# Performance work log

Measured on AMD Instinct MI355X. Metric: run time of the kernel, lower is better.

The kernel has to match this reference:

```python
import jax, jax.numpy as jnp
import numpy as np

P = 64  # number of parameters per grid cell
# torch.combinations(param, 2, with_replacement=True) enumerates (i,j) with i<=j
# in row-major order, which matches np.triu_indices.
IDX_I, IDX_J = np.triu_indices(P)  # each length C = P*(P+1)//2 = 2080


def setup_inputs() -> dict:
    key = jax.random.key(0)
    k1, k2 = jax.random.split(key)
    # [B, G1, G2, P]
    param_tensor = jax.random.normal(k1, (32, 64, 64, P), dtype=jnp.float32)
    # [G1, G2, C]
    coeffs = jax.random.normal(k2, (64, 64, len(IDX_I)), dtype=jnp.float32)
    return {"param_tensor": param_tensor, "coeffs": coeffs}


def reference(param_tensor, coeffs):
    # Pairwise products with replacement: p_i * p_j for i <= j  -> [B,G1,G2,C]
    pair = param_tensor[..., IDX_I] * param_tensor[..., IDX_J]
    # Per-cell weighted sum over combinations, then sum over the 2D grid -> [B]
    cell = jnp.einsum('bijc,ijc->bij', pair, coeffs)
    return cell.sum(axis=(1, 2))
```

## Files before the change

kernel.cpp:

```cpp
#include <hip/hip_runtime.h>

#define NP     64
#define NC     2080
#define NCELLS 4096
#define NB     32
#define CELLS_PER_BLOCK 4
#define BLOCKS (NCELLS / CELLS_PER_BLOCK)
#define CSTRIDE 2112

typedef short bf16x8  __attribute__((ext_vector_type(8)));
typedef short short4v __attribute__((ext_vector_type(4)));
typedef float f32x16  __attribute__((ext_vector_type(16)));

__device__ __forceinline__ short f2bf(float f) {
  unsigned u = __float_as_uint(f);
  u += 0x7fffu + ((u >> 16) & 1u);
  return (short)(u >> 16);
}

__global__ __launch_bounds__(256, 4) void poly_mfma_kernel(
    const float* __restrict__ param,
    const float* __restrict__ coeffs,
    float* __restrict__ ws) {
  __shared__ short scoefh[CELLS_PER_BLOCK][CSTRIDE];
  __shared__ float sred[CELLS_PER_BLOCK][NB];

  const int tid  = threadIdx.x;
  const int wave = tid >> 6;
  const int lane = tid & 63;
  const int lo5  = lane & 31;
  const int hi   = lane >> 5;
  const int cellbase = blockIdx.x * CELLS_PER_BLOCK;
  const int cell = cellbase + wave;

  {
    const float4* gsrc =
        reinterpret_cast<const float4*>(coeffs + (size_t)cellbase * NC);
#pragma unroll
    for (int k = 0; k < 9; ++k) {
      const int idx = tid + k * 256;
      if (idx < (CELLS_PER_BLOCK * NC) / 4) {
        const int cl = idx / 520;
        const int q  = idx - cl * 520;
        const float4 v = gsrc[idx];
        short4v h;
        h[0] = f2bf(v.x); h[1] = f2bf(v.y);
        h[2] = f2bf(v.z); h[3] = f2bf(v.w);
        *reinterpret_cast<short4v*>(&scoefh[cl][4 * q]) = h;
      }
    }
  }

  const float* pb = param + ((size_t)lo5 * NCELLS + cell) * NP;
  bf16x8 afrag[4];
#pragma unroll
  for (int ks = 0; ks < 4; ++ks) {
#pragma unroll
    for (int eh = 0; eh < 2; ++eh) {
      const int i0 = ks * 16 + 4 * hi + 8 * eh;
      const float4 v = *reinterpret_cast<const float4*>(pb + i0);
      afrag[ks][eh * 4 + 0] = f2bf(v.x);
      afrag[ks][eh * 4 + 1] = f2bf(v.y);
      afrag[ks][eh * 4 + 2] = f2bf(v.z);
      afrag[ks][eh * 4 + 3] = f2bf(v.w);
    }
  }

  __syncthreads();

  float pepi0[16], pepi1[16];
#pragma unroll
  for (int r = 0; r < 16; ++r) {
    const int b = (r & 3) + 8 * (r >> 2) + 4 * hi;
    const float* pe = param + ((size_t)b * NCELLS + cell) * NP;
    pepi0[r] = pe[lo5];
    pepi1[r] = pe[lo5 + 32];
  }

  const short* sw = &scoefh[wave][0];
  f32x16 acc0, acc1;
#pragma unroll
  for (int r = 0; r < 16; ++r) { acc0[r] = 0.f; acc1[r] = 0.f; }

#pragma unroll
  for (int ks = 0; ks < 4; ++ks) {
    bf16x8 b0, b1;
#pragma unroll
    for (int e = 0; e < 8; ++e) {
      const int i = ks * 16 + 4 * hi + (e & 3) + 8 * (e >> 2);
      const int cbase = i * (127 - i) / 2;
      const short v0 = sw[cbase + lo5];
      const short v1 = sw[cbase + lo5 + 32];
      b0[e] = (lo5 >= i) ? v0 : (short)0;
      b1[e] = (lo5 + 32 >= i) ? v1 : (short)0;
    }
    acc0 = __builtin_amdgcn_mfma_f32_32x32x16_bf16(afrag[ks], b0, acc0, 0, 0, 0);
    acc1 = __builtin_amdgcn_mfma_f32_32x32x16_bf16(afrag[ks], b1, acc1, 0, 0, 0);
  }

  float dacc[16];
#pragma unroll
  for (int r = 0; r < 16; ++r)
    dacc[r] = fmaf(acc0[r], pepi0[r], acc1[r] * pepi1[r]);

#pragma unroll
  for (int r = 0; r < 16; ++r) {
    float v = dacc[r];
    v += __shfl_xor(v, 1, 64);
    v += __shfl_xor(v, 2, 64);
    v += __shfl_xor(v, 4, 64);
    v += __shfl_xor(v, 8, 64);
    v += __shfl_xor(v, 16, 64);
    dacc[r] = v;
  }
  if (lo5 == 0) {
#pragma unroll
    for (int r = 0; r < 16; ++r) {
      const int b = (r & 3) + 8 * (r >> 2) + 4 * hi;
      sred[wave][b] = dacc[r];
    }
  }
  __syncthreads();
  if (tid < NB) {
    ws[(size_t)tid * BLOCKS + blockIdx.x] =
        sred[0][tid] + sred[1][tid] + sred[2][tid] + sred[3][tid];
  }
}

__global__ void poly_reduce_kernel(const float* __restrict__ ws,
                                   float* __restrict__ out) {
  const int b = blockIdx.x;
  const int tid = threadIdx.x;
  const float4 v =
      reinterpret_cast<const float4*>(ws + (size_t)b * BLOCKS)[tid];
  float s = (v.x + v.y) + (v.z + v.w);
#pragma unroll
  for (int off = 1; off <= 32; off <<= 1) s += __shfl_xor(s, off, 64);
  __shared__ float sp[4];
  if ((tid & 63) == 0) sp[tid >> 6] = s;
  __syncthreads();
  if (tid == 0) out[b] = (sp[0] + sp[1]) + (sp[2] + sp[3]);
}

extern "C" void kernel_launch(void* const* d_in, const int* in_sizes, int n_in,
                              void* d_out, int out_size, void* d_ws,
                              size_t ws_size, hipStream_t stream) {
  const float* param = (const float*)d_in[0];
  const float* coeffs = (const float*)d_in[1];
  float* out = (float*)d_out;
  float* ws = (float*)d_ws;

  hipLaunchKernelGGL(poly_mfma_kernel, dim3(BLOCKS), dim3(256), 0, stream,
                     param, coeffs, ws);
  hipLaunchKernelGGL(poly_reduce_kernel, dim3(NB), dim3(256), 0, stream, ws,
                     out);
}
```

Before: 22.30 us.

## Store coefficients as swizzled transposed upper-triangular matrix and use DPP reductions

Each wave now loads only its own cell's coefficients into a zero-initialised, XOR-swizzled 64x64 transposed bf16 tile in shared memory, placing each element by inverting the triangular index with a sqrt. This lets the MFMA B operand be fetched with two vector LDS reads per fragment, replacing eight scalar reads plus masking, and removes the block barrier before the compute loop. The cross-lane reduction switches from shfl_xor to DPP row rotations plus a ds_swizzle. The costs are extra zero-fill stores, scattered 2-byte LDS writes with per-element index math, and correctness that relies on the wave-local zero and fill completing before the reads.

Result: faster. 21.69 us, median of 3 (-2.8%).

```diff
diff --git a/kernel.cpp b/kernel.cpp
--- a/kernel.cpp
+++ b/kernel.cpp
@@ -6,7 +6,6 @@
 #define NB     32
 #define CELLS_PER_BLOCK 4
 #define BLOCKS (NCELLS / CELLS_PER_BLOCK)
-#define CSTRIDE 2112
 
 typedef short bf16x8  __attribute__((ext_vector_type(8)));
 typedef short short4v __attribute__((ext_vector_type(4)));
@@ -18,11 +17,19 @@
   return (short)(u >> 16);
 }
 
+__device__ __forceinline__ int swz(int j, int i) { return i ^ ((j & 15) << 2); }
+
+template <int CTRL>
+__device__ __forceinline__ float ror_add(float v) {
+  int t = __builtin_amdgcn_update_dpp(0, __float_as_int(v), CTRL, 0xf, 0xf, true);
+  return v + __int_as_float(t);
+}
+
 __global__ __launch_bounds__(256, 4) void poly_mfma_kernel(
     const float* __restrict__ param,
     const float* __restrict__ coeffs,
     float* __restrict__ ws) {
-  __shared__ short scoefh[CELLS_PER_BLOCK][CSTRIDE];
+  __shared__ __align__(16) short scoefT[CELLS_PER_BLOCK][NP][NP];
   __shared__ float sred[CELLS_PER_BLOCK][NB];
 
   const int tid  = threadIdx.x;
@@ -30,23 +37,38 @@
   const int lane = tid & 63;
   const int lo5  = lane & 31;
   const int hi   = lane >> 5;
-  const int cellbase = blockIdx.x * CELLS_PER_BLOCK;
-  const int cell = cellbase + wave;
+  const int cell = blockIdx.x * CELLS_PER_BLOCK + wave;
+
+  {
+    int4* z = reinterpret_cast<int4*>(&scoefT[wave][0][0]);
+    const int4 zero = {0, 0, 0, 0};
+#pragma unroll
+    for (int k = 0; k < 8; ++k) z[k * 64 + lane] = zero;
+  }
 
   {
     const float4* gsrc =
-        reinterpret_cast<const float4*>(coeffs + (size_t)cellbase * NC);
+        reinterpret_cast<const float4*>(coeffs + (size_t)cell * NC);
 #pragma unroll
     for (int k = 0; k < 9; ++k) {
-      const int idx = tid + k * 256;
-      if (idx < (CELLS_PER_BLOCK * NC) / 4) {
-        const int cl = idx / 520;
-        const int q  = idx - cl * 520;
+      const int idx = k * 64 + lane;
+      if (idx < NC / 4) {
         const float4 v = gsrc[idx];
-        short4v h;
-        h[0] = f2bf(v.x); h[1] = f2bf(v.y);
-        h[2] = f2bf(v.z); h[3] = f2bf(v.w);
-        *reinterpret_cast<short4v*>(&scoefh[cl][4 * q]) = h;
+        const int c = idx * 4;
+        const float fs = sqrtf((float)(16641 - 8 * c));
+        int i = (int)((129.0f - fs) * 0.5f);
+        int bi = 64 * i - ((i * (i - 1)) >> 1);
+        if (c < bi) { --i; bi -= (64 - i); }
+        else if (c >= bi + (64 - i)) { bi += (64 - i); ++i; }
+        int off = c - bi;
+        const float vals[4] = {v.x, v.y, v.z, v.w};
+#pragma unroll
+        for (int d = 0; d < 4; ++d) {
+          const int j = i + off;
+          scoefT[wave][j][swz(j, i)] = f2bf(vals[d]);
+          ++off;
+          if (off == 64 - i) { ++i; off = 0; }
+        }
       }
     }
   }
@@ -66,8 +88,6 @@
     }
   }
 
-  __syncthreads();
-
   float pepi0[16], pepi1[16];
 #pragma unroll
   for (int r = 0; r < 16; ++r) {
@@ -77,47 +97,38 @@
     pepi1[r] = pe[lo5 + 32];
   }
 
-  const short* sw = &scoefh[wave][0];
+  const short* swT = &scoefT[wave][0][0];
+  const int jb0 = lo5 * NP;
+  const int jb1 = (lo5 + 32) * NP;
   f32x16 acc0, acc1;
 #pragma unroll
   for (int r = 0; r < 16; ++r) { acc0[r] = 0.f; acc1[r] = 0.f; }
 
 #pragma unroll
   for (int ks = 0; ks < 4; ++ks) {
-    bf16x8 b0, b1;
-#pragma unroll
-    for (int e = 0; e < 8; ++e) {
-      const int i = ks * 16 + 4 * hi + (e & 3) + 8 * (e >> 2);
-      const int cbase = i * (127 - i) / 2;
-      const short v0 = sw[cbase + lo5];
-      const short v1 = sw[cbase + lo5 + 32];
-      b0[e] = (lo5 >= i) ? v0 : (short)0;
-      b1[e] = (lo5 + 32 >= i) ? v1 : (short)0;
-    }
+    const int ia = ks * 16 + 4 * hi;
+    const int ib = ia + 8;
+    const short4v a0 = *reinterpret_cast<const short4v*>(swT + jb0 + swz(lo5, ia));
+    const short4v a1 = *reinterpret_cast<const short4v*>(swT + jb0 + swz(lo5, ib));
+    const short4v c0 = *reinterpret_cast<const short4v*>(swT + jb1 + swz(lo5, ia));
+    const short4v c1 = *reinterpret_cast<const short4v*>(swT + jb1 + swz(lo5, ib));
+    const bf16x8 b0 = __builtin_shufflevector(a0, a1, 0, 1, 2, 3, 4, 5, 6, 7);
+    const bf16x8 b1 = __builtin_shufflevector(c0, c1, 0, 1, 2, 3, 4, 5, 6, 7);
     acc0 = __builtin_amdgcn_mfma_f32_32x32x16_bf16(afrag[ks], b0, acc0, 0, 0, 0);
     acc1 = __builtin_amdgcn_mfma_f32_32x32x16_bf16(afrag[ks], b1, acc1, 0, 0, 0);
   }
 
-  float dacc[16];
-#pragma unroll
-  for (int r = 0; r < 16; ++r)
-    dacc[r] = fmaf(acc0[r], pepi0[r], acc1[r] * pepi1[r]);
-
 #pragma unroll
   for (int r = 0; r < 16; ++r) {
-    float v = dacc[r];
-    v += __shfl_xor(v, 1, 64);
-    v += __shfl_xor(v, 2, 64);
-    v += __shfl_xor(v, 4, 64);
-    v += __shfl_xor(v, 8, 64);
-    v += __shfl_xor(v, 16, 64);
-    dacc[r] = v;
-  }
-  if (lo5 == 0) {
-#pragma unroll
-    for (int r = 0; r < 16; ++r) {
+    float v = fmaf(acc0[r], pepi0[r], acc1[r] * pepi1[r]);
+    v = ror_add<0x121>(v);
+    v = ror_add<0x122>(v);
+    v = ror_add<0x124>(v);
+    v = ror_add<0x128>(v);
+    v += __int_as_float(__builtin_amdgcn_ds_swizzle(__float_as_int(v), 0x401F));
+    if (lo5 == 0) {
       const int b = (r & 3) + 8 * (r >> 2) + 4 * hi;
-      sred[wave][b] = dacc[r];
+      sred[wave][b] = v;
     }
   }
   __syncthreads();
```
